# Kernel tuning notes

Hardware: AMD Instinct MI355X
Metric: run time of the kernel (lower is better)

## Reference

```python
import jax, jax.numpy as jnp
import numpy as np

N_NODES = 100000
N_EDGES = 3200000
N_IN = 128
N_OUT = 64
ITERATIONS = 150
LEAK = 0.01


def _mml_activation(v):
    # piecewise: leaky below 0, Michaelis-Menten-like saturation above 0.5
    v = jnp.where(v < 0, v * LEAK, v)
    safe = jnp.where(v > 0.5, v, 1.0)  # avoid div-by-zero on untaken branch
    return jnp.where(v > 0.5, 1.0 - 0.25 / safe, v)


def setup_inputs() -> dict:
    key = jax.random.key(0)
    ks = jax.random.split(key, 9)
    x = jax.random.normal(ks[0], (1, N_IN), dtype=jnp.float32)
    in_weights = jnp.ones((N_IN,), jnp.float32)  # inputAmplitude * ones
    # weights init: 0.1 + 0.1*U, sign flipped for inhibitory reactions
    mag = 0.1 + 0.1 * jax.random.uniform(ks[1], (N_EDGES,), dtype=jnp.float32)
    sign = jnp.where(jax.random.bernoulli(ks[2], 0.5, (N_EDGES,)), 1.0, -1.0)
    rec_weights = mag * sign
    biases = 0.001 * jnp.ones((N_NODES,), jnp.float32)
    out_weights = jnp.ones((N_OUT,), jnp.float32)  # projectionAmplitude * ones
    in_indices = jax.random.randint(ks[3], (N_IN,), 0, N_NODES, dtype=jnp.int32)
    edge_rows = jax.random.randint(ks[4], (N_EDGES,), 0, N_NODES, dtype=jnp.int32)
    edge_cols = jax.random.randint(ks[5], (N_EDGES,), 0, N_NODES, dtype=jnp.int32)
    out_indices = jax.random.randint(ks[6], (N_OUT,), 0, N_NODES, dtype=jnp.int32)
    return {"x": x, "in_weights": in_weights, "rec_weights": rec_weights,
            "biases": biases, "out_weights": out_weights,
            "in_indices": in_indices, "edge_rows": edge_rows,
            "edge_cols": edge_cols, "out_indices": out_indices}


def reference(x, in_weights, rec_weights, biases, out_weights,
              in_indices, edge_rows, edge_cols, out_indices):
    # input projection: scatter weighted inputs into node vector [N_NODES]
    node_in = jnp.zeros((N_NODES,), x.dtype).at[in_indices].set(in_weights * x[0])
    b_in = node_in + biases

    def step(y, _):
        # sparse matvec A @ y: gather sources, weight, scatter-add to rows
        s = jax.ops.segment_sum(rec_weights * y[edge_cols], edge_rows,
                                num_segments=N_NODES)
        return _mml_activation(s + b_in), None

    y0 = jnp.zeros((N_NODES,), x.dtype)
    y, _ = jax.lax.scan(step, y0, None, length=ITERATIONS)
    # output projection: gather + scale -> [1, N_OUT]
    return (out_weights * y[out_indices])[None, :]
```

## Files before the change

### kernel.cpp

```cpp
#include <hip/hip_runtime.h>

#define N_NODES 100000
#define N_EDGES 3200000
#define N_IN    128
#define N_OUT   64
#define ITERS   150
#define LEAK    0.01f

#define NBLK    256
#define NT      960
#define GROUPS  240
#define RPB     391
#define SCAN_CHUNK 1024
#define SCAN_NBLK  98
#define ARRSTR  16
#define YSTR    100096
#define NBUF    150

__device__ __forceinline__ float mml(float v) {
    v = (v < 0.0f) ? v * LEAK : v;
    if (v > 0.5f) v = 1.0f - 0.25f / v;
    return v;
}

__global__ void k_binit(const float* __restrict__ biases, float* __restrict__ b_in) {
    int i = blockIdx.x * blockDim.x + threadIdx.x;
    if (i < N_NODES) b_in[i] = biases[i];
}

__global__ void k_scatter_in(const float* __restrict__ x,
                             const float* __restrict__ in_w,
                             const int*   __restrict__ in_idx,
                             const float* __restrict__ biases,
                             float* __restrict__ b_in) {
    int k = threadIdx.x;
    if (k < N_IN) {
        int idx = in_idx[k];
        bool last = true;
        for (int j = k + 1; j < N_IN; ++j)
            if (in_idx[j] == idx) { last = false; break; }
        if (last) b_in[idx] = biases[idx] + in_w[k] * x[k];
    }
}

__global__ void k_y0(const float* __restrict__ b_in, float* __restrict__ y0) {
    int i = blockIdx.x * blockDim.x + threadIdx.x;
    if (i < N_NODES) y0[i] = mml(b_in[i]);
}

__global__ void k_hist(const int* __restrict__ rows, int* __restrict__ counts) {
    int i = blockIdx.x * blockDim.x + threadIdx.x;
    int stride = gridDim.x * blockDim.x;
    for (; i < N_EDGES; i += stride) atomicAdd(&counts[rows[i]], 1);
}

__global__ void k_scan1(const int* __restrict__ counts, int* __restrict__ rp,
                        int* __restrict__ blockSums) {
    __shared__ int sm[SCAN_CHUNK];
    int t = threadIdx.x;
    int i = blockIdx.x * SCAN_CHUNK + t;
    int v = (i < N_NODES) ? counts[i] : 0;
    sm[t] = v;
    __syncthreads();
    for (int off = 1; off < SCAN_CHUNK; off <<= 1) {
        int add = (t >= off) ? sm[t - off] : 0;
        __syncthreads();
        sm[t] += add;
        __syncthreads();
    }
    if (i <= N_NODES) rp[i] = sm[t] - v;
    if (t == SCAN_CHUNK - 1) blockSums[blockIdx.x] = sm[t];
}

__global__ void k_scan2(int* __restrict__ blockSums) {
    __shared__ int sm[128];
    int t = threadIdx.x;
    int v = (t < SCAN_NBLK) ? blockSums[t] : 0;
    sm[t] = v;
    __syncthreads();
    for (int off = 1; off < 128; off <<= 1) {
        int add = (t >= off) ? sm[t - off] : 0;
        __syncthreads();
        sm[t] += add;
        __syncthreads();
    }
    if (t < SCAN_NBLK) blockSums[t] = sm[t] - v;
}

__global__ void k_scan3(int* __restrict__ rp, const int* __restrict__ blockSums,
                        int* __restrict__ next) {
    int i = blockIdx.x * SCAN_CHUNK + threadIdx.x;
    if (i <= N_NODES) {
        int val = rp[i] + blockSums[blockIdx.x];
        rp[i] = val;
        if (i < N_NODES) next[i] = val;
    }
}

__global__ void k_scatter_edges(const int* __restrict__ rows, const int* __restrict__ cols,
                                const float* __restrict__ w,
                                int* __restrict__ next, int2* __restrict__ csr) {
    int i = blockIdx.x * blockDim.x + threadIdx.x;
    int stride = gridDim.x * blockDim.x;
    for (; i < N_EDGES; i += stride) {
        int r = rows[i];
        int p = atomicAdd(&next[r], 1);
        csr[p] = make_int2(cols[i], __float_as_int(w[i]));
    }
}

template <bool SC1>
__device__ __forceinline__ float row_part(const int2* __restrict__ csr,
                                          const float* __restrict__ ysrc,
                                          int e, const int end) {
    float a0 = 0.f, a1 = 0.f;
    for (; e + 4 < end; e += 8) {
        const int2 c0 = csr[e];
        const int2 c1 = csr[e + 4];
        float y0, y1;
        if (SC1) {
            y0 = __hip_atomic_load(&ysrc[c0.x], __ATOMIC_RELAXED, __HIP_MEMORY_SCOPE_AGENT);
            y1 = __hip_atomic_load(&ysrc[c1.x], __ATOMIC_RELAXED, __HIP_MEMORY_SCOPE_AGENT);
        } else { y0 = ysrc[c0.x]; y1 = ysrc[c1.x]; }
        a0 = fmaf(__int_as_float(c0.y), y0, a0);
        a1 = fmaf(__int_as_float(c1.y), y1, a1);
    }
    if (e < end) {
        const int2 c = csr[e];
        const float yv = SC1 ? __hip_atomic_load(&ysrc[c.x], __ATOMIC_RELAXED,
                                                 __HIP_MEMORY_SCOPE_AGENT)
                             : ysrc[c.x];
        a0 = fmaf(__int_as_float(c.y), yv, a0);
    }
    return a0 + a1;
}

template <bool SC1>
__global__ __launch_bounds__(NT) void k_iterate(
    const int*  __restrict__ rp,
    const int2* __restrict__ csr,
    const float* __restrict__ b_in,
    float* __restrict__ ybufs,
    int* __restrict__ arr,
    const int* __restrict__ out_idx,
    const float* __restrict__ out_w,
    float* __restrict__ out,
    int nbuf)
{
    const int b = blockIdx.x, t = threadIdx.x;
    const int gq = t >> 2, j = t & 3;
    const int row0 = b * RPB;
    const int row_end = (row0 + RPB < N_NODES) ? row0 + RPB : N_NODES;
    const int nrows = row_end - row0;

    int beg1 = 0, end1 = 0, beg2 = 0, end2 = 0;
    float bi1 = 0.f, bi2 = 0.f;
    const int r1 = row0 + gq, r2 = row0 + gq + GROUPS;
    const bool h1 = (gq < nrows), h2 = (gq + GROUPS < nrows);
    if (h1) { beg1 = rp[r1] + j; end1 = rp[r1 + 1]; bi1 = b_in[r1]; }
    if (h2) { beg2 = rp[r2] + j; end2 = rp[r2 + 1]; bi2 = b_in[r2]; }

    for (int it = 1; it <= ITERS - 1; ++it) {
        const float* ysrc = ybufs + (size_t)((it - 1) % nbuf) * YSTR;
        float*       ydst = ybufs + (size_t)(it % nbuf) * YSTR;

        float acc1 = h1 ? row_part<SC1>(csr, ysrc, beg1, end1) : 0.f;
        float acc2 = h2 ? row_part<SC1>(csr, ysrc, beg2, end2) : 0.f;

        acc1 += __shfl_xor(acc1, 1); acc1 += __shfl_xor(acc1, 2);
        acc2 += __shfl_xor(acc2, 1); acc2 += __shfl_xor(acc2, 2);
        if (j == 0) {
            if (h1)
                __hip_atomic_store(&ydst[r1], mml(bi1 + acc1),
                                   __ATOMIC_RELAXED, __HIP_MEMORY_SCOPE_AGENT);
            if (h2)
                __hip_atomic_store(&ydst[r2], mml(bi2 + acc2),
                                   __ATOMIC_RELAXED, __HIP_MEMORY_SCOPE_AGENT);
        }
        asm volatile("s_waitcnt vmcnt(0)" ::: "memory");
        __builtin_amdgcn_s_barrier();
        if (t == 0)
            __hip_atomic_store(&arr[b * ARRSTR], it, __ATOMIC_RELAXED,
                               __HIP_MEMORY_SCOPE_AGENT);
        if (t < NBLK) {
            while (__hip_atomic_load(&arr[t * ARRSTR], __ATOMIC_RELAXED,
                                     __HIP_MEMORY_SCOPE_AGENT) < it)
                __builtin_amdgcn_s_sleep(2);
        }
        __syncthreads();
    }

    if (b == 0 && t < N_OUT) {
        const float* yfin = ybufs + (size_t)((ITERS - 1) % nbuf) * YSTR;
        out[t] = out_w[t] * __hip_atomic_load(&yfin[out_idx[t]],
                   __ATOMIC_RELAXED, __HIP_MEMORY_SCOPE_AGENT);
    }
}

extern "C" void kernel_launch(void* const* d_in, const int* in_sizes, int n_in,
                              void* d_out, int out_size, void* d_ws, size_t ws_size,
                              hipStream_t stream) {
    const float* x      = (const float*)d_in[0];
    const float* in_w   = (const float*)d_in[1];
    const float* rec_w  = (const float*)d_in[2];
    const float* biases = (const float*)d_in[3];
    const float* out_w  = (const float*)d_in[4];
    const int*   in_idx = (const int*)d_in[5];
    const int*   e_rows = (const int*)d_in[6];
    const int*   e_cols = (const int*)d_in[7];
    const int*   out_idx= (const int*)d_in[8];
    float* out = (float*)d_out;

    char* ws = (char*)d_ws;
    float* b_in    = (float*)ws;
    int*   rp      = (int*)(b_in + N_NODES);
    int*   counts  = rp + (N_NODES + 64);
    int*   blockSums = counts + N_NODES;
    int*   arr     = blockSums + 128;
    size_t off = (size_t)((char*)(arr + NBLK * ARRSTR) - ws);
    off = (off + 255) & ~(size_t)255;
    int2* csr = (int2*)(ws + off);
    size_t off2 = off + (size_t)N_EDGES * sizeof(int2);
    off2 = (off2 + 255) & ~(size_t)255;
    float* ybufs = (float*)(ws + off2);

    long long avail = ((long long)ws_size - (long long)off2) /
                      (long long)(YSTR * sizeof(float));
    int nbuf, sc1mode;
    if (avail >= NBUF) { nbuf = NBUF; sc1mode = 0; }
    else               { nbuf = 2;    sc1mode = 1; }

    hipMemsetAsync(counts, 0, N_NODES * sizeof(int), stream);
    hipMemsetAsync(arr, 0, NBLK * ARRSTR * sizeof(int), stream);

    k_binit<<<391, 256, 0, stream>>>(biases, b_in);
    k_scatter_in<<<1, 128, 0, stream>>>(x, in_w, in_idx, biases, b_in);
    k_y0<<<391, 256, 0, stream>>>(b_in, ybufs);

    k_hist<<<1024, 256, 0, stream>>>(e_rows, counts);
    k_scan1<<<SCAN_NBLK, SCAN_CHUNK, 0, stream>>>(counts, rp, blockSums);
    k_scan2<<<1, 128, 0, stream>>>(blockSums);
    k_scan3<<<SCAN_NBLK, SCAN_CHUNK, 0, stream>>>(rp, blockSums, counts);
    k_scatter_edges<<<1024, 256, 0, stream>>>(e_rows, e_cols, rec_w, counts, csr);

    int*   rp_a   = rp;
    int2*  csr_a  = csr;
    float* bin_a  = b_in;
    float* yb_a   = ybufs;
    int*   arr_a  = arr;
    const int*   oidx_a = out_idx;
    const float* ow_a   = out_w;
    float* out_a  = out;
    void* args[] = { &rp_a, &csr_a, &bin_a, &yb_a, &arr_a,
                     &oidx_a, &ow_a, &out_a, &nbuf };
    void* kfn = sc1mode ? (void*)k_iterate<true> : (void*)k_iterate<false>;
    hipLaunchCooperativeKernel(kfn, dim3(NBLK), dim3(NT), args, 0, stream);
}
```

Before: 3.179 ms.

## Pad CSR rows to multiples of eight and exit early on period-2 convergence

Each CSR row is padded to a multiple of 8 entries with zero-weight entries, so the per-thread gather loop has a fixed trip count and no tail. The two rows a thread owns are now processed in one interleaved loop to expose more memory-level parallelism. Each iteration, every block compares its new state bitwise with the state from two iterations earlier and publishes a flag in a per-block ring. When all blocks report a match, the kernel stops and picks the buffer whose parity matches the final iteration, skipping the remaining sweeps. The cost is a larger CSR buffer plus a memset to zero it, and extra flag traffic in the grid barrier.

```diff
diff --git a/kernel.cpp b/kernel.cpp
--- a/kernel.cpp
+++ b/kernel.cpp
@@ -14,8 +14,10 @@
 #define SCAN_CHUNK 1024
 #define SCAN_NBLK  98
 #define ARRSTR  16
+#define CRS     16
 #define YSTR    100096
 #define NBUF    150
+#define CSRMAX  (N_EDGES + 8 * N_NODES)
 
 __device__ __forceinline__ float mml(float v) {
     v = (v < 0.0f) ? v * LEAK : v;
@@ -59,7 +61,7 @@
     __shared__ int sm[SCAN_CHUNK];
     int t = threadIdx.x;
     int i = blockIdx.x * SCAN_CHUNK + t;
-    int v = (i < N_NODES) ? counts[i] : 0;
+    int v = (i < N_NODES) ? ((counts[i] + 7) & ~7) : 0;
     sm[t] = v;
     __syncthreads();
     for (int off = 1; off < SCAN_CHUNK; off <<= 1) {
@@ -110,38 +112,13 @@
 }
 
 template <bool SC1>
-__device__ __forceinline__ float row_part(const int2* __restrict__ csr,
-                                          const float* __restrict__ ysrc,
-                                          int e, const int end) {
-    float a0 = 0.f, a1 = 0.f;
-    for (; e + 4 < end; e += 8) {
-        const int2 c0 = csr[e];
-        const int2 c1 = csr[e + 4];
-        float y0, y1;
-        if (SC1) {
-            y0 = __hip_atomic_load(&ysrc[c0.x], __ATOMIC_RELAXED, __HIP_MEMORY_SCOPE_AGENT);
-            y1 = __hip_atomic_load(&ysrc[c1.x], __ATOMIC_RELAXED, __HIP_MEMORY_SCOPE_AGENT);
-        } else { y0 = ysrc[c0.x]; y1 = ysrc[c1.x]; }
-        a0 = fmaf(__int_as_float(c0.y), y0, a0);
-        a1 = fmaf(__int_as_float(c1.y), y1, a1);
-    }
-    if (e < end) {
-        const int2 c = csr[e];
-        const float yv = SC1 ? __hip_atomic_load(&ysrc[c.x], __ATOMIC_RELAXED,
-                                                 __HIP_MEMORY_SCOPE_AGENT)
-                             : ysrc[c.x];
-        a0 = fmaf(__int_as_float(c.y), yv, a0);
-    }
-    return a0 + a1;
-}
-
-template <bool SC1>
 __global__ __launch_bounds__(NT) void k_iterate(
     const int*  __restrict__ rp,
     const int2* __restrict__ csr,
     const float* __restrict__ b_in,
     float* __restrict__ ybufs,
     int* __restrict__ arr,
+    int* __restrict__ convring,
     const int* __restrict__ out_idx,
     const float* __restrict__ out_w,
     float* __restrict__ out,
@@ -152,46 +129,95 @@
     const int row0 = b * RPB;
     const int row_end = (row0 + RPB < N_NODES) ? row0 + RPB : N_NODES;
     const int nrows = row_end - row0;
-
-    int beg1 = 0, end1 = 0, beg2 = 0, end2 = 0;
-    float bi1 = 0.f, bi2 = 0.f;
     const int r1 = row0 + gq, r2 = row0 + gq + GROUPS;
     const bool h1 = (gq < nrows), h2 = (gq + GROUPS < nrows);
-    if (h1) { beg1 = rp[r1] + j; end1 = rp[r1 + 1]; bi1 = b_in[r1]; }
-    if (h2) { beg2 = rp[r2] + j; end2 = rp[r2 + 1]; bi2 = b_in[r2]; }
-
+
+    int beg1 = 0, n1 = 0, beg2 = 0, n2 = 0;
+    float bi1 = 0.f, bi2 = 0.f;
+    if (h1) { int s = rp[r1]; n1 = (rp[r1 + 1] - s) >> 3; beg1 = s + j; bi1 = b_in[r1]; }
+    if (h2) { int s = rp[r2]; n2 = (rp[r2 + 1] - s) >> 3; beg2 = s + j; bi2 = b_in[r2]; }
+    const int nmax = (n1 > n2) ? n1 : n2;
+
+    int finalbuf = (ITERS - 1) % nbuf;
     for (int it = 1; it <= ITERS - 1; ++it) {
         const float* ysrc = ybufs + (size_t)((it - 1) % nbuf) * YSTR;
         float*       ydst = ybufs + (size_t)(it % nbuf) * YSTR;
-
-        float acc1 = h1 ? row_part<SC1>(csr, ysrc, beg1, end1) : 0.f;
-        float acc2 = h2 ? row_part<SC1>(csr, ysrc, beg2, end2) : 0.f;
+        const float* yp2  = ybufs + (size_t)((it >= 3 ? it - 2 : 0) % nbuf) * YSTR;
+
+        float acc1 = 0.f, acc2 = 0.f;
+        int e1 = beg1, e2 = beg2;
+        for (int k = 0; k < nmax; ++k) {
+            int2 a0, a1, c0, c1;
+            const bool p = (k < n1), q = (k < n2);
+            if (p) { a0 = csr[e1]; a1 = csr[e1 + 4]; }
+            if (q) { c0 = csr[e2]; c1 = csr[e2 + 4]; }
+            float ya0, ya1, yc0, yc1;
+            if (p) {
+                if (SC1) {
+                    ya0 = __hip_atomic_load(&ysrc[a0.x], __ATOMIC_RELAXED, __HIP_MEMORY_SCOPE_AGENT);
+                    ya1 = __hip_atomic_load(&ysrc[a1.x], __ATOMIC_RELAXED, __HIP_MEMORY_SCOPE_AGENT);
+                } else { ya0 = ysrc[a0.x]; ya1 = ysrc[a1.x]; }
+            }
+            if (q) {
+                if (SC1) {
+                    yc0 = __hip_atomic_load(&ysrc[c0.x], __ATOMIC_RELAXED, __HIP_MEMORY_SCOPE_AGENT);
+                    yc1 = __hip_atomic_load(&ysrc[c1.x], __ATOMIC_RELAXED, __HIP_MEMORY_SCOPE_AGENT);
+                } else { yc0 = ysrc[c0.x]; yc1 = ysrc[c1.x]; }
+            }
+            if (p) {
+                acc1 = fmaf(__int_as_float(a0.y), ya0, acc1);
+                acc1 = fmaf(__int_as_float(a1.y), ya1, acc1);
+                e1 += 8;
+            }
+            if (q) {
+                acc2 = fmaf(__int_as_float(c0.y), yc0, acc2);
+                acc2 = fmaf(__int_as_float(c1.y), yc1, acc2);
+                e2 += 8;
+            }
+        }
 
         acc1 += __shfl_xor(acc1, 1); acc1 += __shfl_xor(acc1, 2);
         acc2 += __shfl_xor(acc2, 1); acc2 += __shfl_xor(acc2, 2);
+        int convflag = (!SC1 && it >= 3) ? 1 : 0;
         if (j == 0) {
-            if (h1)
-                __hip_atomic_store(&ydst[r1], mml(bi1 + acc1),
-                                   __ATOMIC_RELAXED, __HIP_MEMORY_SCOPE_AGENT);
-            if (h2)
-                __hip_atomic_store(&ydst[r2], mml(bi2 + acc2),
-                                   __ATOMIC_RELAXED, __HIP_MEMORY_SCOPE_AGENT);
+            if (h1) {
+                float v = mml(bi1 + acc1);
+                __hip_atomic_store(&ydst[r1], v, __ATOMIC_RELAXED, __HIP_MEMORY_SCOPE_AGENT);
+                if (convflag) convflag = (__float_as_int(v) == __float_as_int(yp2[r1]));
+            }
+            if (h2) {
+                float v = mml(bi2 + acc2);
+                __hip_atomic_store(&ydst[r2], v, __ATOMIC_RELAXED, __HIP_MEMORY_SCOPE_AGENT);
+                if (convflag) convflag = convflag && (__float_as_int(v) == __float_as_int(yp2[r2]));
+            }
         }
         asm volatile("s_waitcnt vmcnt(0)" ::: "memory");
-        __builtin_amdgcn_s_barrier();
-        if (t == 0)
-            __hip_atomic_store(&arr[b * ARRSTR], it, __ATOMIC_RELAXED,
-                               __HIP_MEMORY_SCOPE_AGENT);
+        int blockconv = __syncthreads_and(j != 0 || convflag);
+
+        if (t == 0) {
+            __hip_atomic_store(&convring[((it & 3) * NBLK + b) * CRS], blockconv,
+                               __ATOMIC_RELAXED, __HIP_MEMORY_SCOPE_AGENT);
+            asm volatile("s_waitcnt vmcnt(0)" ::: "memory");
+            __hip_atomic_store(&arr[b * ARRSTR], it,
+                               __ATOMIC_RELAXED, __HIP_MEMORY_SCOPE_AGENT);
+        }
+        int cb = 1;
         if (t < NBLK) {
             while (__hip_atomic_load(&arr[t * ARRSTR], __ATOMIC_RELAXED,
                                      __HIP_MEMORY_SCOPE_AGENT) < it)
-                __builtin_amdgcn_s_sleep(2);
-        }
-        __syncthreads();
+                __builtin_amdgcn_s_sleep(1);
+            cb = __hip_atomic_load(&convring[((it & 3) * NBLK + t) * CRS],
+                                   __ATOMIC_RELAXED, __HIP_MEMORY_SCOPE_AGENT);
+        }
+        int allconv = __syncthreads_and(cb != 0);
+        if (allconv) {
+            finalbuf = (((ITERS - 1 - it) & 1) == 0) ? (it % nbuf) : ((it - 1) % nbuf);
+            break;
+        }
     }
 
     if (b == 0 && t < N_OUT) {
-        const float* yfin = ybufs + (size_t)((ITERS - 1) % nbuf) * YSTR;
+        const float* yfin = ybufs + (size_t)finalbuf * YSTR;
         out[t] = out_w[t] * __hip_atomic_load(&yfin[out_idx[t]],
                    __ATOMIC_RELAXED, __HIP_MEMORY_SCOPE_AGENT);
     }
@@ -217,21 +243,25 @@
     int*   counts  = rp + (N_NODES + 64);
     int*   blockSums = counts + N_NODES;
     int*   arr     = blockSums + 128;
-    size_t off = (size_t)((char*)(arr + NBLK * ARRSTR) - ws);
+    int*   convring= arr + NBLK * ARRSTR;
+    size_t off = (size_t)((char*)(convring + 4 * NBLK * CRS) - ws);
     off = (off + 255) & ~(size_t)255;
     int2* csr = (int2*)(ws + off);
-    size_t off2 = off + (size_t)N_EDGES * sizeof(int2);
+    size_t off2 = off + (size_t)CSRMAX * sizeof(int2);
     off2 = (off2 + 255) & ~(size_t)255;
     float* ybufs = (float*)(ws + off2);
 
     long long avail = ((long long)ws_size - (long long)off2) /
                       (long long)(YSTR * sizeof(float));
     int nbuf, sc1mode;
-    if (avail >= NBUF) { nbuf = NBUF; sc1mode = 0; }
-    else               { nbuf = 2;    sc1mode = 1; }
+    if (avail >= 48) {
+        nbuf = (avail >= NBUF) ? NBUF : (int)avail;
+        sc1mode = 0;
+    } else { nbuf = 2; sc1mode = 1; }
 
     hipMemsetAsync(counts, 0, N_NODES * sizeof(int), stream);
-    hipMemsetAsync(arr, 0, NBLK * ARRSTR * sizeof(int), stream);
+    hipMemsetAsync(arr, 0, (NBLK * ARRSTR + 4 * NBLK * CRS) * sizeof(int), stream);
+    hipMemsetAsync(csr, 0, (size_t)CSRMAX * sizeof(int2), stream);
 
     k_binit<<<391, 256, 0, stream>>>(biases, b_in);
     k_scatter_in<<<1, 128, 0, stream>>>(x, in_w, in_idx, biases, b_in);
@@ -248,10 +278,11 @@
     float* bin_a  = b_in;
     float* yb_a   = ybufs;
     int*   arr_a  = arr;
+    int*   cr_a   = convring;
     const int*   oidx_a = out_idx;
     const float* ow_a   = out_w;
     float* out_a  = out;
-    void* args[] = { &rp_a, &csr_a, &bin_a, &yb_a, &arr_a,
+    void* args[] = { &rp_a, &csr_a, &bin_a, &yb_a, &arr_a, &cr_a,
                      &oidx_a, &ow_a, &out_a, &nbuf };
     void* kfn = sc1mode ? (void*)k_iterate<true> : (void*)k_iterate<false>;
     hipLaunchCooperativeKernel(kfn, dim3(NBLK), dim3(NT), args, 0, stream);
```

After: 3.426 ms. 7.8% more time.

## Process block edges as flat stream with LDS atomic row accumulation

Applied to the files above, without the earlier changes.

Replaces the per-row, four-lanes-per-row CSR traversal with a flat pass over every edge a block owns. The local row index is packed into the upper bits of the column word, and partial sums go into a shared-memory accumulator through LDS atomics. Each thread issues 26 independent edge and y loads per batch, which raises memory-level parallelism and removes load imbalance from uneven row lengths. In exchange it adds LDS atomic contention, an extra block barrier per iteration, clamped padding loads, and a fall in block size from 960 to 512 threads.

```diff
diff --git a/kernel.cpp b/kernel.cpp
--- a/kernel.cpp
+++ b/kernel.cpp
@@ -8,14 +8,16 @@
 #define LEAK    0.01f
 
 #define NBLK    256
-#define NT      960
-#define GROUPS  240
+#define NT      512
 #define RPB     391
+#define BD      26
 #define SCAN_CHUNK 1024
 #define SCAN_NBLK  98
 #define ARRSTR  16
 #define YSTR    100096
 #define NBUF    150
+#define COLMASK 0x1FFFF
+#define RSHIFT  17
 
 __device__ __forceinline__ float mml(float v) {
     v = (v < 0.0f) ? v * LEAK : v;
@@ -104,35 +106,10 @@
     int stride = gridDim.x * blockDim.x;
     for (; i < N_EDGES; i += stride) {
         int r = rows[i];
+        int blk = r / RPB;
         int p = atomicAdd(&next[r], 1);
-        csr[p] = make_int2(cols[i], __float_as_int(w[i]));
-    }
-}
-
-template <bool SC1>
-__device__ __forceinline__ float row_part(const int2* __restrict__ csr,
-                                          const float* __restrict__ ysrc,
-                                          int e, const int end) {
-    float a0 = 0.f, a1 = 0.f;
-    for (; e + 4 < end; e += 8) {
-        const int2 c0 = csr[e];
-        const int2 c1 = csr[e + 4];
-        float y0, y1;
-        if (SC1) {
-            y0 = __hip_atomic_load(&ysrc[c0.x], __ATOMIC_RELAXED, __HIP_MEMORY_SCOPE_AGENT);
-            y1 = __hip_atomic_load(&ysrc[c1.x], __ATOMIC_RELAXED, __HIP_MEMORY_SCOPE_AGENT);
-        } else { y0 = ysrc[c0.x]; y1 = ysrc[c1.x]; }
-        a0 = fmaf(__int_as_float(c0.y), y0, a0);
-        a1 = fmaf(__int_as_float(c1.y), y1, a1);
-    }
-    if (e < end) {
-        const int2 c = csr[e];
-        const float yv = SC1 ? __hip_atomic_load(&ysrc[c.x], __ATOMIC_RELAXED,
-                                                 __HIP_MEMORY_SCOPE_AGENT)
-                             : ysrc[c.x];
-        a0 = fmaf(__int_as_float(c.y), yv, a0);
-    }
-    return a0 + a1;
+        csr[p] = make_int2(cols[i] | ((r - blk * RPB) << RSHIFT), __float_as_int(w[i]));
+    }
 }
 
 template <bool SC1>
@@ -147,35 +124,52 @@
     float* __restrict__ out,
     int nbuf)
 {
+    __shared__ float acc[RPB];
     const int b = blockIdx.x, t = threadIdx.x;
-    const int gq = t >> 2, j = t & 3;
     const int row0 = b * RPB;
     const int row_end = (row0 + RPB < N_NODES) ? row0 + RPB : N_NODES;
     const int nrows = row_end - row0;
-
-    int beg1 = 0, end1 = 0, beg2 = 0, end2 = 0;
-    float bi1 = 0.f, bi2 = 0.f;
-    const int r1 = row0 + gq, r2 = row0 + gq + GROUPS;
-    const bool h1 = (gq < nrows), h2 = (gq + GROUPS < nrows);
-    if (h1) { beg1 = rp[r1] + j; end1 = rp[r1 + 1]; bi1 = b_in[r1]; }
-    if (h2) { beg2 = rp[r2] + j; end2 = rp[r2 + 1]; bi2 = b_in[r2]; }
+    const int sbeg = rp[row0];
+    const int send = rp[row_end];
+    const int last = send - 1;
+    const float bi = (t < nrows) ? b_in[row0 + t] : 0.f;
+
+    for (int i = t; i < RPB; i += NT) acc[i] = 0.f;
+    __syncthreads();
 
     for (int it = 1; it <= ITERS - 1; ++it) {
         const float* ysrc = ybufs + (size_t)((it - 1) % nbuf) * YSTR;
         float*       ydst = ybufs + (size_t)(it % nbuf) * YSTR;
 
-        float acc1 = h1 ? row_part<SC1>(csr, ysrc, beg1, end1) : 0.f;
-        float acc2 = h2 ? row_part<SC1>(csr, ysrc, beg2, end2) : 0.f;
-
-        acc1 += __shfl_xor(acc1, 1); acc1 += __shfl_xor(acc1, 2);
-        acc2 += __shfl_xor(acc2, 1); acc2 += __shfl_xor(acc2, 2);
-        if (j == 0) {
-            if (h1)
-                __hip_atomic_store(&ydst[r1], mml(bi1 + acc1),
-                                   __ATOMIC_RELAXED, __HIP_MEMORY_SCOPE_AGENT);
-            if (h2)
-                __hip_atomic_store(&ydst[r2], mml(bi2 + acc2),
-                                   __ATOMIC_RELAXED, __HIP_MEMORY_SCOPE_AGENT);
+        for (int base = sbeg + t; base < send; base += BD * NT) {
+            int2  u[BD];
+            float yv[BD];
+            #pragma unroll
+            for (int k = 0; k < BD; ++k) {
+                const int e = base + k * NT;
+                u[k] = csr[(e < last) ? e : last];
+            }
+            #pragma unroll
+            for (int k = 0; k < BD; ++k) {
+                const int c = u[k].x & COLMASK;
+                yv[k] = SC1 ? __hip_atomic_load(&ysrc[c], __ATOMIC_RELAXED,
+                                                __HIP_MEMORY_SCOPE_AGENT)
+                            : ysrc[c];
+            }
+            #pragma unroll
+            for (int k = 0; k < BD; ++k) {
+                const int e = base + k * NT;
+                const float wk = (e < send) ? __int_as_float(u[k].y) : 0.f;
+                atomicAdd(&acc[u[k].x >> RSHIFT], wk * yv[k]);
+            }
+        }
+        __syncthreads();
+
+        if (t < nrows) {
+            const float v = mml(bi + acc[t]);
+            __hip_atomic_store(&ydst[row0 + t], v,
+                               __ATOMIC_RELAXED, __HIP_MEMORY_SCOPE_AGENT);
+            acc[t] = 0.f;
         }
         asm volatile("s_waitcnt vmcnt(0)" ::: "memory");
         __builtin_amdgcn_s_barrier();
```

After: 4.596 ms. 44.5% more time.
